# Optimization experiments

Measured on AMD Instinct MI355X. Metric: run time of the kernel, lower is better.

The kernel has to match this reference:

```python
import jax, jax.numpy as jnp
import numpy as np

# ---- module constants (from init_kwargs) ----
EMBED_DIM = 384
NUM_HYPEREDGES = 128
TOPK = 64
SPATIAL_SHAPE = (16, 32, 32)  # D, H, W -> N = 16384
SPACING = (2.0, 1.0, 1.0)
SPATIAL_WEIGHT = 0.1
B, N, C = 4, 16 * 32 * 32, EMBED_DIM


def _l2norm(x, axis=-1, eps=1e-12):
    n = jnp.linalg.norm(x, axis=axis, keepdims=True)
    return x / jnp.maximum(n, eps)


def _get_3d_coords():
    D, H, W = SPATIAL_SHAPE
    z = jnp.arange(D, dtype=jnp.float32) * SPACING[0]
    y = jnp.arange(H, dtype=jnp.float32) * SPACING[1]
    x = jnp.arange(W, dtype=jnp.float32) * SPACING[2]
    zz, yy, xx = jnp.meshgrid(z, y, x, indexing='ij')
    return jnp.stack([zz, yy, xx], axis=-1).reshape(-1, 3)  # (N, 3)


def setup_inputs() -> dict:
    key = jax.random.key(0)
    k1, k2 = jax.random.split(key)
    node_features = jax.random.normal(k1, (B, N, C), dtype=jnp.float32)
    class_token = jax.random.normal(k2, (1, 1, C), dtype=jnp.float32)
    temperature = jnp.ones((1,), dtype=jnp.float32) * 0.07
    return {"node_features": node_features, "class_token": class_token, "temperature": temperature}


def reference(node_features, class_token, temperature):
    Ne = NUM_HYPEREDGES
    w = SPATIAL_WEIGHT
    temp = temperature[0]

    nodes_n = _l2norm(node_features)                      # (B, N, C)

    # Step 1: center sampling by semantic similarity to class token
    ct_n = _l2norm(jnp.broadcast_to(class_token, (B, 1, C)))
    scores = jnp.einsum('boc,bnc->bn', ct_n, nodes_n) / temp  # (B, N)
    _, center_idx = jax.lax.top_k(scores, Ne)             # (B, Ne)

    # Gather centers and compute cosine sim of every center vs all nodes
    centers = jnp.take_along_axis(node_features, center_idx[:, :, None], axis=1)  # (B, Ne, C)
    centers_n = _l2norm(centers)
    sem_sim = jnp.einsum('bec,bnc->ben', centers_n, nodes_n) / temp  # (B, Ne, N)

    # Spatial bias (normalized distance from each center voxel)
    coords = _get_3d_coords()                             # (N, 3)
    center_coords = coords[center_idx]                    # (B, Ne, 3)
    diff = coords[None, None, :, :] - center_coords[:, :, None, :]  # (B, Ne, N, 3)
    dist = jnp.linalg.norm(diff, axis=-1)                 # (B, Ne, N)
    dist = dist / (jnp.max(dist, axis=-1, keepdims=True) + 1e-8)
    combined = (1.0 - w) * sem_sim + w * (1.0 - dist)     # (B, Ne, N)

    # Per-hyperedge top-K neighbors -> incidence matrix H (B, N, Ne)
    _, nbr_idx = jax.lax.top_k(combined, TOPK)            # (B, Ne, K)
    b_ix = jnp.arange(B)[:, None, None]
    e_ix = jnp.arange(Ne)[None, :, None]
    Hmat = jnp.zeros((B, N, Ne), dtype=node_features.dtype)
    Hmat = Hmat.at[b_ix, nbr_idx, e_ix].set(1.0)
    return Hmat
```

## Files before the change

kernel.cpp:

```cpp
#include <hip/hip_runtime.h>
#include <math.h>

#define BB 4
#define NN 16384
#define CC 384
#define NE 128
#define KK 64
#define CAP 1024

typedef unsigned short ushort_t;
typedef __attribute__((ext_vector_type(8))) short bf16x8;
typedef __attribute__((ext_vector_type(4))) float f32x4;
#define MFMA(a, b, c) __builtin_amdgcn_mfma_f32_16x16x32_bf16(a, b, c, 0, 0, 0)

__device__ inline unsigned fkey(float f) {
    unsigned b = __float_as_uint(f);
    return (b & 0x80000000u) ? ~b : (b | 0x80000000u);
}
__device__ inline ushort_t bf16rne(float f) {
    unsigned u = __float_as_uint(f);
    unsigned r = u + 0x7FFFu + ((u >> 16) & 1u);
    return (ushort_t)(r >> 16);
}
__device__ inline float bf16tof(ushort_t h) {
    return __uint_as_float(((unsigned)h) << 16);
}
__device__ inline void cvt2(float fa, float fb, unsigned& hp, unsigned& lp) {
    unsigned ua = __float_as_uint(fa), ub = __float_as_uint(fb);
    unsigned ra = ua + 0x8000u, rb = ub + 0x8000u;
    hp = (ra >> 16) | (rb & 0xFFFF0000u);
    float ha = __uint_as_float(ra & 0xFFFF0000u);
    float hb = __uint_as_float(rb & 0xFFFF0000u);
    float la = fa - ha, lb = fb - hb;
    unsigned lra = __float_as_uint(la) + 0x8000u;
    unsigned lrb = __float_as_uint(lb) + 0x8000u;
    lp = (lra >> 16) | (lrb & 0xFFFF0000u);
}

__device__ inline void load_lds16(const ushort_t* g, ushort_t* l) {
    __builtin_amdgcn_global_load_lds(
        (const __attribute__((address_space(1))) unsigned int*)(const void*)g,
        (__attribute__((address_space(3))) unsigned int*)(void*)l, 16, 0, 0);
}

__device__ inline void bin_select4k(const unsigned* hist, int t, int* wsum,
                                    int* sh_bin, int* sh_r, int r) {
    int base = t * 4;
    int c0 = hist[base], c1 = hist[base + 1], c2 = hist[base + 2], c3 = hist[base + 3];
    int csum = c0 + c1 + c2 + c3;
    int lane = t & 63, wid = t >> 6;
    int x = csum;
#pragma unroll
    for (int off = 1; off < 64; off <<= 1) {
        int v = __shfl_down(x, off, 64);
        if (lane + off < 64) x += v;
    }
    if (lane == 0) wsum[wid] = x;
    __syncthreads();
    int after = 0;
    for (int w2 = wid + 1; w2 < 16; ++w2) after += wsum[w2];
    int S = x - csum + after;
    if (S < r && S + c3 >= r) { *sh_bin = base + 3; *sh_r = r - S; }
    S += c3;
    if (S < r && S + c2 >= r) { *sh_bin = base + 2; *sh_r = r - S; }
    S += c2;
    if (S < r && S + c1 >= r) { *sh_bin = base + 1; *sh_r = r - S; }
    S += c1;
    if (S < r && S + c0 >= r) { *sh_bin = base + 0; *sh_r = r - S; }
    __syncthreads();
}

__global__ __launch_bounds__(256) void k_scores(const float* __restrict__ nf,
                                                const float* __restrict__ ct,
                                                unsigned* __restrict__ keys,
                                                float* __restrict__ invn) {
    int wave = threadIdx.x >> 6;
    int lane = threadIdx.x & 63;
    int row  = blockIdx.x * 4 + wave;
    const float* x = nf + (size_t)row * CC;
    float4 a  = ((const float4*)x)[lane];
    float2 c2 = ((const float2*)(x + 256))[lane];
    float4 ta = ((const float4*)ct)[lane];
    float2 tc = ((const float2*)(ct + 256))[lane];
    float ss = a.x*a.x + a.y*a.y + a.z*a.z + a.w*a.w + c2.x*c2.x + c2.y*c2.y;
    float dt = ta.x*a.x + ta.y*a.y + ta.z*a.z + ta.w*a.w + tc.x*c2.x + tc.y*c2.y;
#pragma unroll
    for (int off = 32; off; off >>= 1) {
        ss += __shfl_xor(ss, off, 64);
        dt += __shfl_xor(dt, off, 64);
    }
    if (lane == 0) {
        float inv = 1.0f / fmaxf(sqrtf(ss), 1e-12f);
        invn[row] = inv;
        keys[row] = fkey(dt * inv);
    }
}

__global__ __launch_bounds__(1024) void k_top128(const unsigned* __restrict__ keys,
                                                 const float* __restrict__ nf,
                                                 const float* __restrict__ invn,
                                                 float* __restrict__ meta,
                                                 ushort_t* __restrict__ Ahi,
                                                 ushort_t* __restrict__ Alo) {
    __shared__ unsigned hist[4096];
    __shared__ int wsum[16];
    __shared__ int sh_bin, sh_r;
    __shared__ unsigned cu[NE];
    __shared__ int cil[NE];
    __shared__ unsigned eqk[CAP];
    __shared__ int eqi[CAP];
    __shared__ int cnt_gt, cnt_eq;
    __shared__ int ocid[NE];
    int b = blockIdx.x;
    int t = threadIdx.x;
    const uint4* rowv = (const uint4*)(keys + b * NN);
    if (t == 0) { cnt_gt = 0; cnt_eq = 0; }
    ((uint4*)hist)[t] = make_uint4(0, 0, 0, 0);
    __syncthreads();
    uint4 u0 = rowv[t], u1 = rowv[t + 1024], u2 = rowv[t + 2048], u3 = rowv[t + 3072];
    atomicAdd(&hist[u0.x >> 20], 1u); atomicAdd(&hist[u0.y >> 20], 1u);
    atomicAdd(&hist[u0.z >> 20], 1u); atomicAdd(&hist[u0.w >> 20], 1u);
    atomicAdd(&hist[u1.x >> 20], 1u); atomicAdd(&hist[u1.y >> 20], 1u);
    atomicAdd(&hist[u1.z >> 20], 1u); atomicAdd(&hist[u1.w >> 20], 1u);
    atomicAdd(&hist[u2.x >> 20], 1u); atomicAdd(&hist[u2.y >> 20], 1u);
    atomicAdd(&hist[u2.z >> 20], 1u); atomicAdd(&hist[u2.w >> 20], 1u);
    atomicAdd(&hist[u3.x >> 20], 1u); atomicAdd(&hist[u3.y >> 20], 1u);
    atomicAdd(&hist[u3.z >> 20], 1u); atomicAdd(&hist[u3.w >> 20], 1u);
    __syncthreads();
    bin_select4k(hist, t, wsum, &sh_bin, &sh_r, NE);
    unsigned bin = (unsigned)sh_bin;
    int r = sh_r;
#define EMIT128(uu, nn) { unsigned tb = (uu) >> 20; \
    if (tb > bin) { int p = atomicAdd(&cnt_gt, 1); cu[p] = (uu); cil[p] = (nn); } \
    else if (tb == bin) { int p = atomicAdd(&cnt_eq, 1); if (p < CAP) { eqk[p] = (uu); eqi[p] = (nn); } } }
    EMIT128(u0.x, 4*t+0); EMIT128(u0.y, 4*t+1); EMIT128(u0.z, 4*t+2); EMIT128(u0.w, 4*t+3);
    EMIT128(u1.x, 4096+4*t+0); EMIT128(u1.y, 4096+4*t+1); EMIT128(u1.z, 4096+4*t+2); EMIT128(u1.w, 4096+4*t+3);
    EMIT128(u2.x, 8192+4*t+0); EMIT128(u2.y, 8192+4*t+1); EMIT128(u2.z, 8192+4*t+2); EMIT128(u2.w, 8192+4*t+3);
    EMIT128(u3.x, 12288+4*t+0); EMIT128(u3.y, 12288+4*t+1); EMIT128(u3.z, 12288+4*t+2); EMIT128(u3.w, 12288+4*t+3);
#undef EMIT128
    __syncthreads();
    int ne = cnt_eq < CAP ? cnt_eq : CAP;
    for (int i = t; i < ne; i += 1024) {
        unsigned ki = eqk[i]; int ii = eqi[i], rk = 0;
        for (int j = 0; j < ne; ++j) {
            unsigned kj = eqk[j];
            rk += (kj > ki) || (kj == ki && eqi[j] < ii);
        }
        if (rk < r) { cu[cnt_gt + rk] = ki; cil[cnt_gt + rk] = ii; }
    }
    __syncthreads();
    if (t < NE) {
        unsigned mu = cu[t]; int mi = cil[t], rk = 0;
#pragma unroll 4
        for (int j = 0; j < NE; ++j) {
            unsigned ou = cu[j]; int oi = cil[j];
            rk += (ou > mu) || (ou == mu && oi < mi);
        }
        ocid[rk] = mi;
    }
    __syncthreads();
    if (t < NE) {
        int ci = ocid[t];
        float zc = (float)(ci >> 10) * 2.0f;
        float yc = (float)((ci >> 5) & 31);
        float xc = (float)(ci & 31);
        float mz = fmaxf(zc * zc, (30.f - zc) * (30.f - zc));
        float my = fmaxf(yc * yc, (31.f - yc) * (31.f - yc));
        float mx = fmaxf(xc * xc, (31.f - xc) * (31.f - xc));
        float md = sqrtf(mz + my + mx);
        int be = b * NE + t;
        meta[be * 4 + 0] = zc;
        meta[be * 4 + 1] = yc;
        meta[be * 4 + 2] = xc;
        meta[be * 4 + 3] = 1.0f / (md + 1e-8f);
    }
    {
        int wid2 = t >> 6, lane2 = t & 63;
        for (int e = wid2; e < NE; e += 16) {
            int ci = ocid[e];
            float inv = invn[b * NN + ci];
            const float* src = nf + ((size_t)b * NN + ci) * CC;
            float4 a  = ((const float4*)src)[lane2];
            float2 cv = ((const float2*)(src + 256))[lane2];
            a.x *= inv; a.y *= inv; a.z *= inv; a.w *= inv;
            cv.x *= inv; cv.y *= inv;
            ushort4 h4; ushort2 h2;
            h4.x = bf16rne(a.x); h4.y = bf16rne(a.y); h4.z = bf16rne(a.z); h4.w = bf16rne(a.w);
            h2.x = bf16rne(cv.x); h2.y = bf16rne(cv.y);
            ushort4 l4; ushort2 l2;
            l4.x = bf16rne(a.x - bf16tof(h4.x)); l4.y = bf16rne(a.y - bf16tof(h4.y));
            l4.z = bf16rne(a.z - bf16tof(h4.z)); l4.w = bf16rne(a.w - bf16tof(h4.w));
            l2.x = bf16rne(cv.x - bf16tof(h2.x)); l2.y = bf16rne(cv.y - bf16tof(h2.y));
            ushort_t* dh = Ahi + ((size_t)b * NE + e) * CC;
            ushort_t* dl = Alo + ((size_t)b * NE + e) * CC;
            ((ushort4*)dh)[lane2] = h4;
            ((ushort2*)(dh + 256))[lane2] = h2;
            ((ushort4*)dl)[lane2] = l4;
            ((ushort2*)(dl + 256))[lane2] = l2;
        }
    }
}

__global__ __launch_bounds__(256, 4) void k_gemm(const float* __restrict__ nf,
                                                 const ushort_t* __restrict__ Ahi,
                                                 const ushort_t* __restrict__ Alo,
                                                 const float* __restrict__ invn,
                                                 const float* __restrict__ meta,
                                                 const float* __restrict__ temp,
                                                 unsigned* __restrict__ outk) {
    __shared__ ushort_t Ah[4 * 128 * 8], Al[4 * 128 * 8];
    __shared__ ushort_t Bh[4][66][8], Bl[4][66][8];
    __shared__ float ms[NE * 4];
    __shared__ float invs_s[64];
    int b  = blockIdx.y;
    int n0 = blockIdx.x * 64;
    int t  = threadIdx.x;
    int w = t >> 6, lane = t & 63, quad = lane >> 4, mrow = lane & 15;
    for (int i = t; i < NE * 4; i += 256) ms[i] = meta[b * NE * 4 + i];
    if (t < 64) invs_s[t] = invn[b * NN + n0 + t];
    f32x4 acc[2][4];
#pragma unroll
    for (int i = 0; i < 2; ++i)
#pragma unroll
        for (int j = 0; j < 4; ++j) acc[i][j] = (f32x4)0.f;
    const ushort_t* Abh = Ahi + (size_t)b * NE * CC;
    const ushort_t* Abl = Alo + (size_t)b * NE * CC;
    int q64a = w * 2, q64b = w * 2 + 1;
    int slota = q64a * 64 + lane, slotb = q64b * 64 + lane;
    const ushort_t* gha = Abh + (size_t)(slota & 127) * CC + (slota >> 7) * 8;
    const ushort_t* ghb = Abh + (size_t)(slotb & 127) * CC + (slotb >> 7) * 8;
    const ushort_t* gla = Abl + (size_t)(slota & 127) * CC + (slota >> 7) * 8;
    const ushort_t* glb = Abl + (size_t)(slotb & 127) * CC + (slotb >> 7) * 8;
    ushort_t* ldsAha = &Ah[(q64a * 64) * 8];
    ushort_t* ldsAhb = &Ah[(q64b * 64) * 8];
    ushort_t* ldsAla = &Al[(q64a * 64) * 8];
    ushort_t* ldsAlb = &Al[(q64b * 64) * 8];
    int bn = t >> 2, bk8 = t & 3;
    const float* bs = nf + ((size_t)b * NN + n0 + bn) * CC + bk8 * 8;
    float4 pBa = ((const float4*)bs)[0];
    float4 pBb = ((const float4*)bs)[1];
    for (int kt = 0; kt < CC; kt += 32) {
        __syncthreads();
        load_lds16(gha + kt, ldsAha);
        load_lds16(ghb + kt, ldsAhb);
        load_lds16(gla + kt, ldsAla);
        load_lds16(glb + kt, ldsAlb);
        {
            uint4 ph, pl;
            cvt2(pBa.x, pBa.y, ph.x, pl.x);
            cvt2(pBa.z, pBa.w, ph.y, pl.y);
            cvt2(pBb.x, pBb.y, ph.z, pl.z);
            cvt2(pBb.z, pBb.w, ph.w, pl.w);
            *(uint4*)&Bh[bk8][bn][0] = ph;
            *(uint4*)&Bl[bk8][bn][0] = pl;
        }
        if (kt + 32 < CC) {
            pBa = ((const float4*)(bs + kt + 32))[0];
            pBb = ((const float4*)(bs + kt + 32))[1];
        }
        __syncthreads();
        bf16x8 afh[2], afl[2], bfh[4], bfl[4];
#pragma unroll
        for (int i = 0; i < 2; ++i) {
            int m = w * 32 + i * 16 + mrow;
            afh[i] = *(const bf16x8*)&Ah[(quad * 128 + m) * 8];
            afl[i] = *(const bf16x8*)&Al[(quad * 128 + m) * 8];
        }
#pragma unroll
        for (int j = 0; j < 4; ++j) {
            int n = j * 16 + mrow;
            bfh[j] = *(const bf16x8*)&Bh[quad][n][0];
            bfl[j] = *(const bf16x8*)&Bl[quad][n][0];
        }
#pragma unroll
        for (int i = 0; i < 2; ++i)
#pragma unroll
            for (int j = 0; j < 4; ++j) {
                acc[i][j] = MFMA(afh[i], bfh[j], acc[i][j]);
                acc[i][j] = MFMA(afh[i], bfl[j], acc[i][j]);
                acc[i][j] = MFMA(afl[i], bfh[j], acc[i][j]);
            }
    }
    float scale = 0.9f / temp[0];
#pragma unroll
    for (int j = 0; j < 4; ++j) {
        int nloc = j * 16 + mrow;
        int n = n0 + nloc;
        float invnn = invs_s[nloc];
        float zf = (float)(n >> 10) * 2.0f;
        float yf = (float)((n >> 5) & 31);
        float xf = (float)(n & 31);
#pragma unroll
        for (int i = 0; i < 2; ++i) {
#pragma unroll
            for (int r = 0; r < 4; ++r) {
                int el = w * 32 + i * 16 + quad * 4 + r;
                float zc = ms[el * 4 + 0], yc = ms[el * 4 + 1], xc = ms[el * 4 + 2], ivd = ms[el * 4 + 3];
                float dz = zf - zc, dy = yf - yc, dx = xf - xc;
                float dist = sqrtf(dz * dz + dy * dy + dx * dx);
                float v = scale * invnn * acc[i][j][r] + 0.1f * (1.0f - dist * ivd);
                outk[((size_t)(b * NE + el)) * NN + n] = fkey(v);
            }
        }
    }
}

__global__ __launch_bounds__(512) void k_top64(const unsigned* __restrict__ comb,
                                               unsigned* __restrict__ bmg) {
    __shared__ unsigned hist[4096];
    __shared__ unsigned bm[512];
    __shared__ int wsum[8];
    __shared__ int sh_bin, sh_r;
    __shared__ unsigned eqk[CAP];
    __shared__ int eqi[CAP];
    __shared__ int cnt_eq;
    int be = blockIdx.x;
    int t  = threadIdx.x;
    const uint4* rowv = (const uint4*)(comb + (size_t)be * NN);
    if (t == 0) cnt_eq = 0;
    ((uint4*)hist)[t] = make_uint4(0, 0, 0, 0);
    ((uint4*)hist)[t + 512] = make_uint4(0, 0, 0, 0);
    if (t < 128) ((uint4*)bm)[t] = make_uint4(0, 0, 0, 0);
    __syncthreads();
    uint4 u[8];
#pragma unroll
    for (int i = 0; i < 8; ++i) u[i] = rowv[t + 512 * i];
#pragma unroll
    for (int i = 0; i < 8; ++i) {
        atomicAdd(&hist[u[i].x >> 20], 1u); atomicAdd(&hist[u[i].y >> 20], 1u);
        atomicAdd(&hist[u[i].z >> 20], 1u); atomicAdd(&hist[u[i].w >> 20], 1u);
    }
    __syncthreads();
    {
        int base = t * 8;
        int c[8]; int csum = 0;
#pragma unroll
        for (int i = 0; i < 8; ++i) { c[i] = hist[base + i]; csum += c[i]; }
        int lane = t & 63, wid = t >> 6;
        int x = csum;
#pragma unroll
        for (int off = 1; off < 64; off <<= 1) {
            int v = __shfl_down(x, off, 64);
            if (lane + off < 64) x += v;
        }
        if (lane == 0) wsum[wid] = x;
        __syncthreads();
        int after = 0;
        for (int w2 = wid + 1; w2 < 8; ++w2) after += wsum[w2];
        int S = x - csum + after;
#pragma unroll
        for (int i = 7; i >= 0; --i) {
            if (S < KK && S + c[i] >= KK) { sh_bin = base + i; sh_r = KK - S; }
            S += c[i];
        }
        __syncthreads();
    }
    unsigned bin = (unsigned)sh_bin;
    int r = sh_r;
#define EMIT64(uu, nn) { unsigned tb = (uu) >> 20; \
    if (tb > bin) { atomicOr(&bm[(nn) >> 5], 1u << ((nn) & 31)); } \
    else if (tb == bin) { int p = atomicAdd(&cnt_eq, 1); if (p < CAP) { eqk[p] = (uu); eqi[p] = (nn); } } }
#pragma unroll
    for (int i = 0; i < 8; ++i) {
        int nb = 4 * (t + 512 * i);
        EMIT64(u[i].x, nb + 0); EMIT64(u[i].y, nb + 1);
        EMIT64(u[i].z, nb + 2); EMIT64(u[i].w, nb + 3);
    }
#undef EMIT64
    __syncthreads();
    int ne = cnt_eq < CAP ? cnt_eq : CAP;
    for (int i = t; i < ne; i += 512) {
        unsigned ki = eqk[i]; int ii = eqi[i], rk = 0;
        for (int j = 0; j < ne; ++j) {
            unsigned kj = eqk[j];
            rk += (kj > ki) || (kj == ki && eqi[j] < ii);
        }
        if (rk < r) atomicOr(&bm[ii >> 5], 1u << (ii & 31));
    }
    __syncthreads();
    if (t < 128) ((uint4*)(bmg + (size_t)be * 512))[t] = ((uint4*)bm)[t];
}

__global__ __launch_bounds__(256) void k_expand(const unsigned* __restrict__ bmg,
                                                float* __restrict__ H) {
    __shared__ unsigned wl[256];
    int b  = blockIdx.y;
    int n0 = blockIdx.x * 64;
    int t  = threadIdx.x;
    int w0 = n0 >> 5;
    wl[t] = bmg[((size_t)b * NE + (t >> 1)) * 512 + w0 + (t & 1)];
    __syncthreads();
    float4* dst = (float4*)(H + ((size_t)b * NN + n0) * NE);
#pragma unroll
    for (int i = 0; i < 8; ++i) {
        int flat = t + 256 * i;
        int nl = flat >> 5, f4 = flat & 31;
        int wsel = nl >> 5, bit = nl & 31;
        int e = f4 * 4;
        float4 v;
        v.x = (float)((wl[(e + 0) * 2 + wsel] >> bit) & 1u);
        v.y = (float)((wl[(e + 1) * 2 + wsel] >> bit) & 1u);
        v.z = (float)((wl[(e + 2) * 2 + wsel] >> bit) & 1u);
        v.w = (float)((wl[(e + 3) * 2 + wsel] >> bit) & 1u);
        dst[flat] = v;
    }
}

extern "C" void kernel_launch(void* const* d_in, const int* in_sizes, int n_in,
                              void* d_out, int out_size, void* d_ws, size_t ws_size,
                              hipStream_t stream) {
    const float* nf   = (const float*)d_in[0];
    const float* ct   = (const float*)d_in[1];
    const float* temp = (const float*)d_in[2];
    float* out = (float*)d_out;

    unsigned* keys = (unsigned*)d_ws;
    float* invn    = (float*)(keys + BB * NN);
    float* meta    = invn + BB * NN;
    ushort_t* Ahi  = (ushort_t*)(meta + BB * NE * 4);
    ushort_t* Alo  = Ahi + (size_t)BB * NE * CC;
    unsigned* bmg  = (unsigned*)(Alo + (size_t)BB * NE * CC);

    k_scores <<<BB * NN / 4, 256, 0, stream>>>(nf, ct, keys, invn);
    k_top128 <<<BB, 1024, 0, stream>>>(keys, nf, invn, meta, Ahi, Alo);
    k_gemm   <<<dim3(NN / 64, BB), 256, 0, stream>>>(nf, Ahi, Alo, invn, meta, temp, (unsigned*)out);
    k_top64  <<<BB * NE, 512, 0, stream>>>((const unsigned*)out, bmg);
    k_expand <<<dim3(NN / 64, BB), 256, 0, stream>>>(bmg, out);
}
```

Baseline: 244.1 us.

## Double-buffer k_gemm LDS tiles and widen N tile to 128 columns

The similarity GEMM now processes 128 nodes per block instead of 64, with each wave computing a 64x64 sub-tile, which doubles per-wave MFMA work per LDS load. A and B tiles are double-buffered in LDS, so the next K-slice's async LDS loads and bf16 hi/lo conversion overlap the current slice's MFMAs, with one barrier per step guarded by explicit waitcnt. This trades higher register and LDS use and lower occupancy (launch bounds 256,2) and halves the grid size. A pair of independent histogram atomics is also reordered.

```diff
diff --git a/kernel.cpp b/kernel.cpp
--- a/kernel.cpp
+++ b/kernel.cpp
@@ -125,7 +125,7 @@
     atomicAdd(&hist[u2.x >> 20], 1u); atomicAdd(&hist[u2.y >> 20], 1u);
     atomicAdd(&hist[u2.z >> 20], 1u); atomicAdd(&hist[u2.w >> 20], 1u);
     atomicAdd(&hist[u3.x >> 20], 1u); atomicAdd(&hist[u3.y >> 20], 1u);
-    atomicAdd(&hist[u3.z >> 20], 1u); atomicAdd(&hist[u3.w >> 20], 1u);
+    atomicAdd(&hist[u3.w >> 20], 1u); atomicAdd(&hist[u3.z >> 20], 1u);
     __syncthreads();
     bin_select4k(hist, t, wsum, &sh_bin, &sh_r, NE);
     unsigned bin = (unsigned)sh_bin;
@@ -201,100 +201,124 @@
     }
 }
 
-__global__ __launch_bounds__(256, 4) void k_gemm(const float* __restrict__ nf,
+__global__ __launch_bounds__(256, 2) void k_gemm(const float* __restrict__ nf,
                                                  const ushort_t* __restrict__ Ahi,
                                                  const ushort_t* __restrict__ Alo,
                                                  const float* __restrict__ invn,
                                                  const float* __restrict__ meta,
                                                  const float* __restrict__ temp,
                                                  unsigned* __restrict__ outk) {
-    __shared__ ushort_t Ah[4 * 128 * 8], Al[4 * 128 * 8];
-    __shared__ ushort_t Bh[4][66][8], Bl[4][66][8];
+    __shared__ ushort_t Ah[2][4096], Al[2][4096];
+    __shared__ ushort_t Bh[2][4096], Bl[2][4096];
     __shared__ float ms[NE * 4];
-    __shared__ float invs_s[64];
+    __shared__ float invs_s[128];
     int b  = blockIdx.y;
-    int n0 = blockIdx.x * 64;
+    int n0 = blockIdx.x * 128;
     int t  = threadIdx.x;
     int w = t >> 6, lane = t & 63, quad = lane >> 4, mrow = lane & 15;
+    int wr = w >> 1, wc = w & 1;
     for (int i = t; i < NE * 4; i += 256) ms[i] = meta[b * NE * 4 + i];
-    if (t < 64) invs_s[t] = invn[b * NN + n0 + t];
-    f32x4 acc[2][4];
-#pragma unroll
-    for (int i = 0; i < 2; ++i)
+    if (t < 128) invs_s[t] = invn[b * NN + n0 + t];
+    f32x4 acc[4][4];
+#pragma unroll
+    for (int i = 0; i < 4; ++i)
 #pragma unroll
         for (int j = 0; j < 4; ++j) acc[i][j] = (f32x4)0.f;
     const ushort_t* Abh = Ahi + (size_t)b * NE * CC;
     const ushort_t* Abl = Alo + (size_t)b * NE * CC;
-    int q64a = w * 2, q64b = w * 2 + 1;
-    int slota = q64a * 64 + lane, slotb = q64b * 64 + lane;
-    const ushort_t* gha = Abh + (size_t)(slota & 127) * CC + (slota >> 7) * 8;
-    const ushort_t* ghb = Abh + (size_t)(slotb & 127) * CC + (slotb >> 7) * 8;
-    const ushort_t* gla = Abl + (size_t)(slota & 127) * CC + (slota >> 7) * 8;
-    const ushort_t* glb = Abl + (size_t)(slotb & 127) * CC + (slotb >> 7) * 8;
-    ushort_t* ldsAha = &Ah[(q64a * 64) * 8];
-    ushort_t* ldsAhb = &Ah[(q64b * 64) * 8];
-    ushort_t* ldsAla = &Al[(q64a * 64) * 8];
-    ushort_t* ldsAlb = &Al[(q64b * 64) * 8];
-    int bn = t >> 2, bk8 = t & 3;
-    const float* bs = nf + ((size_t)b * NN + n0 + bn) * CC + bk8 * 8;
-    float4 pBa = ((const float4*)bs)[0];
-    float4 pBb = ((const float4*)bs)[1];
-    for (int kt = 0; kt < CC; kt += 32) {
-        __syncthreads();
-        load_lds16(gha + kt, ldsAha);
-        load_lds16(ghb + kt, ldsAhb);
-        load_lds16(gla + kt, ldsAla);
-        load_lds16(glb + kt, ldsAlb);
-        {
+    const ushort_t* gh0 = Abh + (size_t)lane * CC + w * 8;
+    const ushort_t* gh1 = Abh + (size_t)(64 + lane) * CC + w * 8;
+    const ushort_t* gl0 = Abl + (size_t)lane * CC + w * 8;
+    const ushort_t* gl1 = Abl + (size_t)(64 + lane) * CC + w * 8;
+    int adst0 = 1024 * w, adst1 = 1024 * w + 512;
+    int sb0 = (t & 3) * 128 + (t >> 2);
+    int sb1 = sb0 + 64;
+    const float* bs0 = nf + ((size_t)b * NN + n0 + (t >> 2)) * CC + (t & 3) * 8;
+    const float* bs1 = bs0 + (size_t)64 * CC;
+    float4 p0a = ((const float4*)bs0)[0], p0b = ((const float4*)bs0)[1];
+    float4 p1a = ((const float4*)bs1)[0], p1b = ((const float4*)bs1)[1];
+    load_lds16(gh0, &Ah[0][adst0]);
+    load_lds16(gh1, &Ah[0][adst1]);
+    load_lds16(gl0, &Al[0][adst0]);
+    load_lds16(gl1, &Al[0][adst1]);
+    __builtin_amdgcn_sched_barrier(0);
+    {
+        uint4 ph, pl;
+        cvt2(p0a.x, p0a.y, ph.x, pl.x); cvt2(p0a.z, p0a.w, ph.y, pl.y);
+        cvt2(p0b.x, p0b.y, ph.z, pl.z); cvt2(p0b.z, p0b.w, ph.w, pl.w);
+        *(uint4*)&Bh[0][sb0 * 8] = ph; *(uint4*)&Bl[0][sb0 * 8] = pl;
+        cvt2(p1a.x, p1a.y, ph.x, pl.x); cvt2(p1a.z, p1a.w, ph.y, pl.y);
+        cvt2(p1b.x, p1b.y, ph.z, pl.z); cvt2(p1b.z, p1b.w, ph.w, pl.w);
+        *(uint4*)&Bh[0][sb1 * 8] = ph; *(uint4*)&Bl[0][sb1 * 8] = pl;
+    }
+    p0a = ((const float4*)(bs0 + 32))[0]; p0b = ((const float4*)(bs0 + 32))[1];
+    p1a = ((const float4*)(bs1 + 32))[0]; p1b = ((const float4*)(bs1 + 32))[1];
+    asm volatile("s_waitcnt vmcnt(4) lgkmcnt(0)" ::: "memory");
+    __builtin_amdgcn_s_barrier();
+    __builtin_amdgcn_sched_barrier(0);
+    int cur = 0;
+    for (int ks = 0; ks < 12; ++ks) {
+        int nxt = cur ^ 1;
+        if (ks < 11) {
+            int kt = (ks + 1) * 32;
+            load_lds16(gh0 + kt, &Ah[nxt][adst0]);
+            load_lds16(gh1 + kt, &Ah[nxt][adst1]);
+            load_lds16(gl0 + kt, &Al[nxt][adst0]);
+            load_lds16(gl1 + kt, &Al[nxt][adst1]);
+            __builtin_amdgcn_sched_barrier(0);
             uint4 ph, pl;
-            cvt2(pBa.x, pBa.y, ph.x, pl.x);
-            cvt2(pBa.z, pBa.w, ph.y, pl.y);
-            cvt2(pBb.x, pBb.y, ph.z, pl.z);
-            cvt2(pBb.z, pBb.w, ph.w, pl.w);
-            *(uint4*)&Bh[bk8][bn][0] = ph;
-            *(uint4*)&Bl[bk8][bn][0] = pl;
-        }
-        if (kt + 32 < CC) {
-            pBa = ((const float4*)(bs + kt + 32))[0];
-            pBb = ((const float4*)(bs + kt + 32))[1];
-        }
-        __syncthreads();
-        bf16x8 afh[2], afl[2], bfh[4], bfl[4];
-#pragma unroll
-        for (int i = 0; i < 2; ++i) {
-            int m = w * 32 + i * 16 + mrow;
-            afh[i] = *(const bf16x8*)&Ah[(quad * 128 + m) * 8];
-            afl[i] = *(const bf16x8*)&Al[(quad * 128 + m) * 8];
+            cvt2(p0a.x, p0a.y, ph.x, pl.x); cvt2(p0a.z, p0a.w, ph.y, pl.y);
+            cvt2(p0b.x, p0b.y, ph.z, pl.z); cvt2(p0b.z, p0b.w, ph.w, pl.w);
+            *(uint4*)&Bh[nxt][sb0 * 8] = ph; *(uint4*)&Bl[nxt][sb0 * 8] = pl;
+            cvt2(p1a.x, p1a.y, ph.x, pl.x); cvt2(p1a.z, p1a.w, ph.y, pl.y);
+            cvt2(p1b.x, p1b.y, ph.z, pl.z); cvt2(p1b.z, p1b.w, ph.w, pl.w);
+            *(uint4*)&Bh[nxt][sb1 * 8] = ph; *(uint4*)&Bl[nxt][sb1 * 8] = pl;
+            int kt2 = (ks + 2 < 12) ? (ks + 2) * 32 : 0;
+            p0a = ((const float4*)(bs0 + kt2))[0]; p0b = ((const float4*)(bs0 + kt2))[1];
+            p1a = ((const float4*)(bs1 + kt2))[0]; p1b = ((const float4*)(bs1 + kt2))[1];
+        }
+        bf16x8 afh[4], afl[4], bfh[4], bfl[4];
+#pragma unroll
+        for (int i = 0; i < 4; ++i) {
+            int m = wr * 64 + i * 16 + mrow;
+            afh[i] = *(const bf16x8*)&Ah[cur][(quad * 128 + m) * 8];
+            afl[i] = *(const bf16x8*)&Al[cur][(quad * 128 + m) * 8];
         }
 #pragma unroll
         for (int j = 0; j < 4; ++j) {
-            int n = j * 16 + mrow;
-            bfh[j] = *(const bf16x8*)&Bh[quad][n][0];
-            bfl[j] = *(const bf16x8*)&Bl[quad][n][0];
-        }
-#pragma unroll
-        for (int i = 0; i < 2; ++i)
+            int n = wc * 64 + j * 16 + mrow;
+            bfh[j] = *(const bf16x8*)&Bh[cur][(quad * 128 + n) * 8];
+            bfl[j] = *(const bf16x8*)&Bl[cur][(quad * 128 + n) * 8];
+        }
+#pragma unroll
+        for (int i = 0; i < 4; ++i)
 #pragma unroll
             for (int j = 0; j < 4; ++j) {
                 acc[i][j] = MFMA(afh[i], bfh[j], acc[i][j]);
                 acc[i][j] = MFMA(afh[i], bfl[j], acc[i][j]);
                 acc[i][j] = MFMA(afl[i], bfh[j], acc[i][j]);
             }
+        if (ks < 11) {
+            asm volatile("s_waitcnt vmcnt(4) lgkmcnt(0)" ::: "memory");
+            __builtin_amdgcn_s_barrier();
+            __builtin_amdgcn_sched_barrier(0);
+        }
+        cur = nxt;
     }
     float scale = 0.9f / temp[0];
 #pragma unroll
     for (int j = 0; j < 4; ++j) {
-        int nloc = j * 16 + mrow;
+        int nloc = wc * 64 + j * 16 + mrow;
         int n = n0 + nloc;
         float invnn = invs_s[nloc];
         float zf = (float)(n >> 10) * 2.0f;
         float yf = (float)((n >> 5) & 31);
         float xf = (float)(n & 31);
 #pragma unroll
-        for (int i = 0; i < 2; ++i) {
+        for (int i = 0; i < 4; ++i) {
 #pragma unroll
             for (int r = 0; r < 4; ++r) {
-                int el = w * 32 + i * 16 + quad * 4 + r;
+                int el = wr * 64 + i * 16 + quad * 4 + r;
                 float zc = ms[el * 4 + 0], yc = ms[el * 4 + 1], xc = ms[el * 4 + 2], ivd = ms[el * 4 + 3];
                 float dz = zf - zc, dy = yf - yc, dx = xf - xc;
                 float dist = sqrtf(dz * dz + dy * dy + dx * dx);
@@ -423,7 +447,7 @@
 
     k_scores <<<BB * NN / 4, 256, 0, stream>>>(nf, ct, keys, invn);
     k_top128 <<<BB, 1024, 0, stream>>>(keys, nf, invn, meta, Ahi, Alo);
-    k_gemm   <<<dim3(NN / 64, BB), 256, 0, stream>>>(nf, Ahi, Alo, invn, meta, temp, (unsigned*)out);
+    k_gemm   <<<dim3(NN / 128, BB), 256, 0, stream>>>(nf, Ahi, Alo, invn, meta, temp, (unsigned*)out);
     k_top64  <<<BB * NE, 512, 0, stream>>>((const unsigned*)out, bmg);
     k_expand <<<dim3(NN / 64, BB), 256, 0, stream>>>(bmg, out);
 }
```

Result: faster. 234.4 us (median of 2 runs) (-3.9%).
